# Performance work log

Hardware: AMD Instinct MI355X
Metric: run time of the kernel (lower is better)

Reference implementation:

```python
import jax, jax.numpy as jnp
import numpy as np

H = 1024        # hidden_size
NH = 16         # num heads
HD = H // NH    # head dim = 64
B, S = 2, 2048


def _linear_params(key, fan_in, fan_out):
    k1, k2 = jax.random.split(key)
    bound = 1.0 / np.sqrt(fan_in)
    w = jax.random.uniform(k1, (fan_in, fan_out), jnp.float32, -bound, bound)
    b = jax.random.uniform(k2, (fan_out,), jnp.float32, -bound, bound)
    return w, b


def setup_inputs() -> dict:
    key = jax.random.key(0)
    ks = jax.random.split(key, 10)
    hidden_states = jax.random.normal(ks[0], (B, S, H), jnp.float32)
    topic_states = jax.random.normal(ks[1], (B, H), jnp.float32)
    attention_mask = jnp.zeros((B, 1, 1, S), jnp.float32)
    Wq, bq = _linear_params(ks[2], H, H)
    Wk, bk = _linear_params(ks[3], H, H)
    Wv, bv = _linear_params(ks[4], H, H)
    Wtp, btp = _linear_params(ks[5], H, H)
    Wta, bta = _linear_params(ks[6], H, H)
    Wd, bd = _linear_params(ks[7], H, H)
    ln_g = jnp.ones((H,), jnp.float32)
    ln_b = jnp.zeros((H,), jnp.float32)
    return {
        "hidden_states": hidden_states, "topic_states": topic_states,
        "attention_mask": attention_mask,
        "Wq": Wq, "bq": bq, "Wk": Wk, "bk": bk, "Wv": Wv, "bv": bv,
        "Wtp": Wtp, "btp": btp, "Wta": Wta, "bta": bta,
        "Wd": Wd, "bd": bd, "ln_g": ln_g, "ln_b": ln_b,
    }


def reference(hidden_states, topic_states, attention_mask,
              Wq, bq, Wk, bk, Wv, bv, Wtp, btp, Wta, bta, Wd, bd, ln_g, ln_b):
    # topic gating: two linears on [B,H], broadcast over seq
    topic_proj = topic_states @ Wtp + btp
    topic_att = topic_proj @ Wta + bta                     # [B,H]
    gate = jax.nn.sigmoid(topic_att)[:, None, :]           # [B,1,H]

    q = hidden_states @ Wq + bq                            # [B,S,H]
    k = (hidden_states @ Wk + bk) * gate                   # sigmoid-gated keys
    v = hidden_states @ Wv + bv

    def split_heads(x):  # [B,S,H] -> [B,NH,S,HD]
        return x.reshape(B, S, NH, HD).transpose(0, 2, 1, 3)

    qh, kh, vh = split_heads(q), split_heads(k), split_heads(v)

    scores = jnp.einsum('bhqd,bhkd->bhqk', qh, kh) / np.sqrt(HD).astype(np.float32)
    scores = scores + attention_mask                       # additive mask
    probs = jax.nn.softmax(scores, axis=-1)                # dropout = identity (eval)
    ctx = jnp.einsum('bhqk,bhkd->bhqd', probs, vh)
    ctx = ctx.transpose(0, 2, 1, 3).reshape(B, S, H)

    out = ctx @ Wd + bd                                    # dense + (eval) dropout
    x = out + hidden_states                                # residual
    mu = jnp.mean(x, axis=-1, keepdims=True)
    var = jnp.mean(jnp.square(x - mu), axis=-1, keepdims=True)
    return (x - mu) * jax.lax.rsqrt(var + 1e-5) * ln_g + ln_b
```

## Files before the change

kernel.cpp:

```cpp
#include <hip/hip_runtime.h>

typedef unsigned short u16;
typedef unsigned int   u32;
typedef __attribute__((ext_vector_type(4)))  float f32x4;
typedef __attribute__((ext_vector_type(16))) float f32x16;
typedef __attribute__((ext_vector_type(8)))  __bf16 bf16x8;
typedef __attribute__((ext_vector_type(8)))  u16  u16x8;
typedef __attribute__((ext_vector_type(4)))  u16  u16x4;

#define HDIM 1024
#define SEQ  2048
#define NB   2
#define MROWS 4096
#define QSCALE 0.18033688011111793f
#define LOG2E  1.4426950408889634f
#define TOPK 64
#define TOPC 16

__device__ __forceinline__ u16 f2bf(float f) {
  u32 u = __float_as_uint(f);
  u32 r = u + 0x7FFFu + ((u >> 16) & 1u);
  return (u16)(r >> 16);
}

__device__ __forceinline__ u32 pkbf(float a, float b) {
  union { __bf16 h[2]; u32 w; } u;
  u.h[0] = (__bf16)a; u.h[1] = (__bf16)b;
  return u.w;
}

__device__ __forceinline__ void gload_lds16(const void* gp, void* lp) {
  __builtin_amdgcn_global_load_lds(
      (const __attribute__((address_space(1))) void*)gp,
      (__attribute__((address_space(3))) void*)lp, 16, 0, 0);
}

__global__ void wt_bf16_kernel(const float* __restrict__ w0, const float* __restrict__ w1,
                               const float* __restrict__ w2, const float* __restrict__ w3,
                               u16* __restrict__ out) {
  const float* W = (blockIdx.z == 0) ? w0 : (blockIdx.z == 1) ? w1 : (blockIdx.z == 2) ? w2 : w3;
  u16* Wt = out + (size_t)blockIdx.z * HDIM * HDIM;
  __shared__ float t[32][33];
  const int k0 = blockIdx.x * 32, n0 = blockIdx.y * 32;
  const int tx = threadIdx.x, ty = threadIdx.y;
#pragma unroll
  for (int j = 0; j < 32; j += 8)
    t[ty + j][tx] = W[(size_t)(k0 + ty + j) * HDIM + n0 + tx];
  __syncthreads();
#pragma unroll
  for (int j = 0; j < 32; j += 8)
    Wt[(size_t)(n0 + ty + j) * HDIM + k0 + tx] = f2bf(t[tx][ty + j]);
}

__global__ void cvt_bf16_kernel(const float* __restrict__ in, u16* __restrict__ out) {
  const size_t i = (size_t)blockIdx.x * 256 + threadIdx.x;
  f32x4 v = *(const f32x4*)(in + i * 4);
  u16x4 o;
#pragma unroll
  for (int e = 0; e < 4; ++e) o[e] = f2bf(v[e]);
  *(u16x4*)(out + i * 4) = o;
}

__global__ void topic_partial_kernel(const float* __restrict__ in, const float* __restrict__ W,
                                     float* __restrict__ part) {
  const int c = blockIdx.x;
  const int b = blockIdx.y;
  const int t = threadIdx.x;
  const float* inb = in + b * HDIM + c * TOPK;
  f32x4 acc = {};
#pragma unroll 8
  for (int k = 0; k < TOPK; ++k) {
    const f32x4 w4 = *(const f32x4*)(W + (size_t)(c * TOPK + k) * HDIM + t * 4);
    acc += inb[k] * w4;
  }
  *(f32x4*)(part + ((size_t)(b * TOPC + c)) * HDIM + t * 4) = acc;
}

__global__ void topic_reduce_kernel(const float* __restrict__ part, const float* __restrict__ bias,
                                    float* __restrict__ out, int sigmoid_mode) {
  const int b = blockIdx.y;
  const int n = blockIdx.x * 256 + threadIdx.x;
  float s = bias[n];
#pragma unroll
  for (int c = 0; c < TOPC; ++c) s += part[((size_t)(b * TOPC + c)) * HDIM + n];
  out[b * HDIM + n] = sigmoid_mode ? (1.f / (1.f + __expf(-s))) : s;
}

template <int MODE>
__global__ __launch_bounds__(256, 2)
void gemm_kernel(const u16* __restrict__ A, const u16* __restrict__ Wt,
                 const float* __restrict__ b0, const float* __restrict__ b1,
                 const float* __restrict__ b2, const float* __restrict__ gate,
                 const float* __restrict__ resid,
                 u16* __restrict__ outb, float* __restrict__ outf) {
  const int n0 = blockIdx.x * 128;
  const int m0 = blockIdx.y * 128;
  const int z = blockIdx.z;
  const u16* W = Wt + (size_t)z * (HDIM * HDIM);
  const float* bias = (MODE == 0) ? (z == 0 ? b0 : (z == 1 ? b1 : b2)) : b0;

  __shared__ __align__(16) u16 Alds[128 * 64];
  __shared__ __align__(16) u16 Blds[128 * 64];

  const int tid = threadIdx.x;
  const int lane = tid & 63;
  const int w = tid >> 6;
  const int wm = w >> 1, wn = w & 1;
  const int srow = tid >> 3, sslot = tid & 7;

  f32x4 acc[4][4] = {};

  for (int k0 = 0; k0 < HDIM; k0 += 64) {
    __syncthreads();
#pragma unroll
    for (int j = 0; j < 4; ++j) {
      const int row = j * 32 + srow;
      const int gs = (sslot ^ (row & 7)) * 8;
      gload_lds16(A + (size_t)(m0 + row) * HDIM + k0 + gs, Alds + j * 2048 + w * 512);
      gload_lds16(W + (size_t)(n0 + row) * HDIM + k0 + gs, Blds + j * 2048 + w * 512);
    }
    __syncthreads();
#pragma unroll
    for (int kk = 0; kk < 2; ++kk) {
      const int slot = ((((kk << 2) + (lane >> 4)) ^ (lane & 7)) << 3);
      bf16x8 af[4], bfr[4];
#pragma unroll
      for (int i = 0; i < 4; ++i) {
        af[i]  = *(const bf16x8*)(&Alds[(wm * 64 + i * 16 + (lane & 15)) * 64 + slot]);
        bfr[i] = *(const bf16x8*)(&Blds[(wn * 64 + i * 16 + (lane & 15)) * 64 + slot]);
      }
#pragma unroll
      for (int i = 0; i < 4; ++i)
#pragma unroll
        for (int jn = 0; jn < 4; ++jn)
          acc[i][jn] = __builtin_amdgcn_mfma_f32_16x16x32_bf16(af[i], bfr[jn], acc[i][jn], 0, 0, 0);
    }
  }

  const int rbase = (lane >> 4) << 2;
#pragma unroll
  for (int i = 0; i < 4; ++i) {
#pragma unroll
    for (int jn = 0; jn < 4; ++jn) {
      const int n = n0 + wn * 64 + jn * 16 + (lane & 15);
      const float bv = bias[n];
#pragma unroll
      for (int r = 0; r < 4; ++r) {
        const int m = m0 + wm * 64 + i * 16 + rbase + r;
        float v = acc[i][jn][r] + bv;
        if (MODE == 0) {
          if (z == 0) v *= QSCALE;
          if (z == 1) v *= gate[(m >> 11) * HDIM + n];
          outb[(size_t)z * MROWS * HDIM + (size_t)m * HDIM + n] = f2bf(v);
        } else {
          v += resid[(size_t)m * HDIM + n];
          outf[(size_t)m * HDIM + n] = v;
        }
      }
    }
  }
}

__global__ __launch_bounds__(256, 2)
void attn_kernel(const u16* __restrict__ Q, const u16* __restrict__ K,
                 const u16* __restrict__ V, const float* __restrict__ mask,
                 u16* __restrict__ O) {
  const int q0 = blockIdx.x * 128;
  const int h = blockIdx.y;
  const int b = blockIdx.z;
  const size_t base = ((size_t)b * SEQ) * HDIM + h * 64;
  const int tid = threadIdx.x, lane = tid & 63, w = tid >> 6;
  const int hh = lane >> 5;
  const int ql = lane & 31;
  const int srow = tid >> 3, sslot = tid & 7;

  __shared__ __align__(16) u16 Kss[2][64 * 64];
  __shared__ __align__(16) u16 Vts[2][64 * 64];

  bf16x8 Qf[4];
  {
    const u16* qp = Q + base + (size_t)(q0 + w * 32 + ql) * HDIM;
#pragma unroll
    for (int ds = 0; ds < 4; ++ds)
      Qf[ds] = *(const bf16x8*)(qp + ds * 16 + hh * 8);
  }

  float m_run = -1e30f, l_run = 0.f;
  f32x16 accA = {}, accB = {};

  {
#pragma unroll
    for (int c = 0; c < 2; ++c) {
      const int i2 = c * 4 + w;
      const int row = i2 * 8 + (lane >> 3);
      const int sl = lane & 7;
      gload_lds16(K + base + (size_t)row * HDIM + ((sl ^ (row & 7)) * 8),
                  &Kss[0][i2 * 512]);
    }
    u16x8 vr[2];
#pragma unroll
    for (int jj = 0; jj < 2; ++jj)
      vr[jj] = *(const u16x8*)(V + base + (size_t)(jj * 32 + srow) * HDIM + sslot * 8);
#pragma unroll
    for (int jj = 0; jj < 2; ++jj) {
      const int kr = jj * 32 + srow;
#pragma unroll
      for (int e = 0; e < 8; ++e) {
        const int d = sslot * 8 + e;
        Vts[0][d * 64 + ((((kr >> 3) ^ (d & 7) ^ ((d >> 3) & 7))) << 3) + (kr & 7)] = vr[jj][e];
      }
    }
  }
  __syncthreads();

  for (int t = 0; t < SEQ / 64; ++t) {
    const int cur = t & 1;
    const int kvt0 = t * 64;
    u16x8 vr[2];
    if (t + 1 < SEQ / 64) {
#pragma unroll
      for (int jj = 0; jj < 2; ++jj)
        vr[jj] = *(const u16x8*)(V + base + (size_t)(kvt0 + 64 + jj * 32 + srow) * HDIM + sslot * 8);
#pragma unroll
      for (int c = 0; c < 2; ++c) {
        const int i2 = c * 4 + w;
        const int row = i2 * 8 + (lane >> 3);
        const int sl = lane & 7;
        gload_lds16(K + base + (size_t)(kvt0 + 64 + row) * HDIM + ((sl ^ (row & 7)) * 8),
                    &Kss[cur ^ 1][i2 * 512]);
      }
    }

    f32x16 sv[2] = {{}, {}};
    __builtin_amdgcn_s_setprio(1);
#pragma unroll
    for (int ds = 0; ds < 4; ++ds) {
      const int xo = (((ds * 2 + hh) ^ (ql & 7)) << 3);
      const bf16x8 kf0 = *(const bf16x8*)(&Kss[cur][(ql) * 64 + xo]);
      const bf16x8 kf1 = *(const bf16x8*)(&Kss[cur][(32 + ql) * 64 + xo]);
      sv[0] = __builtin_amdgcn_mfma_f32_32x32x16_bf16(kf0, Qf[ds], sv[0], 0, 0, 0);
      sv[1] = __builtin_amdgcn_mfma_f32_32x32x16_bf16(kf1, Qf[ds], sv[1], 0, 0, 0);
    }
    __builtin_amdgcn_s_setprio(0);

    f32x4 m4[2][4];
    {
      const float* mrow = mask + (size_t)b * SEQ + kvt0 + hh * 4;
#pragma unroll
      for (int g = 0; g < 4; ++g) {
        m4[0][g] = *(const f32x4*)(mrow + g * 8);
        m4[1][g] = *(const f32x4*)(mrow + 32 + g * 8);
      }
    }
    f32x16 s_[2];
#pragma unroll
    for (int kvb = 0; kvb < 2; ++kvb)
#pragma unroll
      for (int j = 0; j < 16; ++j)
        s_[kvb][j] = fmaf(m4[kvb][j >> 2][j & 3], LOG2E, sv[kvb][j]);

    float t8[8];
#pragma unroll
    for (int j = 0; j < 8; ++j)
      t8[j] = fmaxf(fmaxf(s_[0][j], s_[0][j + 8]), fmaxf(s_[1][j], s_[1][j + 8]));
    float t4a = fmaxf(t8[0], t8[1]), t4b = fmaxf(t8[2], t8[3]);
    float t4c = fmaxf(t8[4], t8[5]), t4d = fmaxf(t8[6], t8[7]);
    float mx = fmaxf(fmaxf(t4a, t4b), fmaxf(t4c, t4d));
    mx = fmaxf(mx, __shfl_xor(mx, 32));

    if (!__all(mx <= m_run + 8.f)) {
      const float mnew = fmaxf(m_run, mx);
      const float corr = __builtin_amdgcn_exp2f(m_run - mnew);
      m_run = mnew;
      l_run *= corr;
#pragma unroll
      for (int j = 0; j < 16; ++j) {
        const float cj = __shfl(corr, (j & 3) + 8 * (j >> 2) + 4 * hh);
        accA[j] *= cj; accB[j] *= cj;
      }
    }

    f32x16 p_[2];
#pragma unroll
    for (int kvb = 0; kvb < 2; ++kvb)
#pragma unroll
      for (int j = 0; j < 16; ++j)
        p_[kvb][j] = __builtin_amdgcn_exp2f(s_[kvb][j] - m_run);
    {
      float r8[8];
#pragma unroll
      for (int j = 0; j < 8; ++j)
        r8[j] = (p_[0][j] + p_[0][j + 8]) + (p_[1][j] + p_[1][j + 8]);
      float ra = (r8[0] + r8[1]) + (r8[2] + r8[3]);
      float rb = (r8[4] + r8[5]) + (r8[6] + r8[7]);
      float rs = ra + rb;
      rs += __shfl_xor(rs, 32);
      l_run += rs;
    }

    __builtin_amdgcn_s_setprio(1);
#pragma unroll
    for (int kvb = 0; kvb < 2; ++kvb) {
#pragma unroll
      for (int s2 = 0; s2 < 2; ++s2) {
        const u32 a0 = pkbf(p_[kvb][s2 * 8 + 0], p_[kvb][s2 * 8 + 1]);
        const u32 a1 = pkbf(p_[kvb][s2 * 8 + 2], p_[kvb][s2 * 8 + 3]);
        const u32 b0v = pkbf(p_[kvb][s2 * 8 + 4], p_[kvb][s2 * 8 + 5]);
        const u32 b1v = pkbf(p_[kvb][s2 * 8 + 6], p_[kvb][s2 * 8 + 7]);
        const u32 sd0 = hh ? a0 : b0v, sd1 = hh ? a1 : b1v;
        const u32 r0 = (u32)__shfl_xor((int)sd0, 32);
        const u32 r1 = (u32)__shfl_xor((int)sd1, 32);
        union { u32 u[4]; bf16x8 v; } pu;
        pu.u[0] = hh ? r0 : a0;  pu.u[1] = hh ? r1 : a1;
        pu.u[2] = hh ? b0v : r0; pu.u[3] = hh ? b1v : r1;
        const int ks = kvb * 4 + s2 * 2 + hh;
#pragma unroll
        for (int dt = 0; dt < 2; ++dt) {
          const int d = dt * 32 + ql;
          const bf16x8 vf = *(const bf16x8*)(
              &Vts[cur][d * 64 + ((ks ^ (d & 7) ^ ((d >> 3) & 7)) << 3)]);
          if (dt == 0) accA = __builtin_amdgcn_mfma_f32_32x32x16_bf16(pu.v, vf, accA, 0, 0, 0);
          else         accB = __builtin_amdgcn_mfma_f32_32x32x16_bf16(pu.v, vf, accB, 0, 0, 0);
        }
      }
    }
    __builtin_amdgcn_s_setprio(0);

    if (t + 1 < SEQ / 64) {
#pragma unroll
      for (int jj = 0; jj < 2; ++jj) {
        const int kr = jj * 32 + srow;
#pragma unroll
        for (int e = 0; e < 8; ++e) {
          const int d = sslot * 8 + e;
          Vts[cur ^ 1][d * 64 + ((((kr >> 3) ^ (d & 7) ^ ((d >> 3) & 7))) << 3) + (kr & 7)] = vr[jj][e];
        }
      }
    }
    __syncthreads();
  }

  const float linv = 1.f / l_run;
#pragma unroll
  for (int j = 0; j < 16; ++j) {
    const int rq = (j & 3) + 8 * (j >> 2) + 4 * hh;
    const float lj = __shfl(linv, rq);
    const size_t orow = base + (size_t)(q0 + w * 32 + rq) * HDIM;
    O[orow + ql]      = f2bf(accA[j] * lj);
    O[orow + 32 + ql] = f2bf(accB[j] * lj);
  }
}

__global__ void ln_kernel(const float* __restrict__ x, const float* __restrict__ g,
                          const float* __restrict__ bb, float* __restrict__ out) {
  const int row = blockIdx.x;
  const int tid = threadIdx.x;
  const f32x4 v = *(const f32x4*)(x + (size_t)row * HDIM + tid * 4);
  float s = v[0] + v[1] + v[2] + v[3];
  float s2 = v[0] * v[0] + v[1] * v[1] + v[2] * v[2] + v[3] * v[3];
#pragma unroll
  for (int o = 1; o < 64; o <<= 1) { s += __shfl_xor(s, o); s2 += __shfl_xor(s2, o); }
  __shared__ float rs[4], rs2[4];
  if ((tid & 63) == 0) { rs[tid >> 6] = s; rs2[tid >> 6] = s2; }
  __syncthreads();
  s = rs[0] + rs[1] + rs[2] + rs[3];
  s2 = rs2[0] + rs2[1] + rs2[2] + rs2[3];
  const float mu = s * (1.f / HDIM);
  const float var = s2 * (1.f / HDIM) - mu * mu;
  const float inv = rsqrtf(var + 1e-5f);
  f32x4 o4;
#pragma unroll
  for (int e = 0; e < 4; ++e) {
    const int c = tid * 4 + e;
    o4[e] = (v[e] - mu) * inv * g[c] + bb[c];
  }
  *(f32x4*)(out + (size_t)row * HDIM + tid * 4) = o4;
}

extern "C" void kernel_launch(void* const* d_in, const int* in_sizes, int n_in,
                              void* d_out, int out_size, void* d_ws, size_t ws_size,
                              hipStream_t stream) {
  const float* hidden = (const float*)d_in[0];
  const float* topic  = (const float*)d_in[1];
  const float* mask   = (const float*)d_in[2];
  const float* Wq  = (const float*)d_in[3];  const float* bq  = (const float*)d_in[4];
  const float* Wk  = (const float*)d_in[5];  const float* bk  = (const float*)d_in[6];
  const float* Wv  = (const float*)d_in[7];  const float* bv  = (const float*)d_in[8];
  const float* Wtp = (const float*)d_in[9];  const float* btp = (const float*)d_in[10];
  const float* Wta = (const float*)d_in[11]; const float* bta = (const float*)d_in[12];
  const float* Wd  = (const float*)d_in[13]; const float* bd  = (const float*)d_in[14];
  const float* lng = (const float*)d_in[15]; const float* lnb = (const float*)d_in[16];
  float* out = (float*)d_out;

  char* ws = (char*)d_ws;
  u16* hs_bf  = (u16*)(ws);
  u16* WtAll  = (u16*)(ws + (size_t)(8u << 20));
  u16* qkv    = (u16*)(ws + (size_t)(16u << 20));
  u16* ctx    = (u16*)(ws + (size_t)(40u << 20));
  float* xbuf = (float*)(ws + (size_t)(16u << 20));
  float* tproj = (float*)(ws + (size_t)(48u << 20));
  float* tgate = (float*)(ws + (size_t)(48u << 20) + 8192);
  float* tpart = (float*)(ws + (size_t)(16u << 20));

  wt_bf16_kernel<<<dim3(32, 32, 4), dim3(32, 8), 0, stream>>>(Wq, Wk, Wv, Wd, WtAll);
  cvt_bf16_kernel<<<4096, 256, 0, stream>>>(hidden, hs_bf);
  topic_partial_kernel<<<dim3(TOPC, NB), 256, 0, stream>>>(topic, Wtp, tpart);
  topic_reduce_kernel<<<dim3(4, NB), 256, 0, stream>>>(tpart, btp, tproj, 0);
  topic_partial_kernel<<<dim3(TOPC, NB), 256, 0, stream>>>(tproj, Wta, tpart);
  topic_reduce_kernel<<<dim3(4, NB), 256, 0, stream>>>(tpart, bta, tgate, 1);
  gemm_kernel<0><<<dim3(8, 32, 3), 256, 0, stream>>>(hs_bf, WtAll, bq, bk, bv, tgate,
                                                     nullptr, qkv, nullptr);
  attn_kernel<<<dim3(16, 16, NB), 256, 0, stream>>>(qkv, qkv + (size_t)MROWS * HDIM,
                                                    qkv + 2 * (size_t)MROWS * HDIM, mask, ctx);
  gemm_kernel<1><<<dim3(8, 32, 1), 256, 0, stream>>>(ctx, WtAll + 3 * (size_t)HDIM * HDIM,
                                                     bd, nullptr, nullptr, nullptr, hidden,
                                                     nullptr, xbuf);
  ln_kernel<<<4096, 256, 0, stream>>>(xbuf, lng, lnb, out);
}
```

Before: 165.4 us.

## Split attention KV range in two with a combine kernel for more blocks

The attention kernel gains a SPLIT template mode that processes half of the key/value sequence per block, doubling the grid from 512 to 1024 blocks. Each block writes unnormalized fp32 accumulators and running max/sum to workspace, and a new combine kernel merges the two halves and emits the bf16 context. The change also raises launch bounds to 4 blocks per CU and drops the setprio hints. It aims to fill more of the GPU's compute units, at the cost of extra fp32 partial traffic (about 32 MB written and read back), one more launch, and possible register spills under the tighter launch bound. The split path only runs when the workspace is at least 81 MB.

```diff
diff --git a/kernel.cpp b/kernel.cpp
--- a/kernel.cpp
+++ b/kernel.cpp
@@ -3,6 +3,7 @@
 typedef unsigned short u16;
 typedef unsigned int   u32;
 typedef __attribute__((ext_vector_type(4)))  float f32x4;
+typedef __attribute__((ext_vector_type(2)))  float f32x2;
 typedef __attribute__((ext_vector_type(16))) float f32x16;
 typedef __attribute__((ext_vector_type(8)))  __bf16 bf16x8;
 typedef __attribute__((ext_vector_type(8)))  u16  u16x8;
@@ -161,13 +162,18 @@
   }
 }
 
-__global__ __launch_bounds__(256, 2)
+template <int SPLIT>
+__global__ __launch_bounds__(256, 4)
 void attn_kernel(const u16* __restrict__ Q, const u16* __restrict__ K,
                  const u16* __restrict__ V, const float* __restrict__ mask,
-                 u16* __restrict__ O) {
+                 u16* __restrict__ O, float* __restrict__ pacc, float* __restrict__ pml) {
   const int q0 = blockIdx.x * 128;
   const int h = blockIdx.y;
-  const int b = blockIdx.z;
+  const int zz = blockIdx.z;
+  const int b = SPLIT ? (zz % NB) : zz;
+  const int half = SPLIT ? (zz / NB) : 0;
+  const int kvs = half * (SEQ / 2);
+  const int NT = SPLIT ? (SEQ / 128) : (SEQ / 64);
   const size_t base = ((size_t)b * SEQ) * HDIM + h * 64;
   const int tid = threadIdx.x, lane = tid & 63, w = tid >> 6;
   const int hh = lane >> 5;
@@ -194,13 +200,13 @@
       const int i2 = c * 4 + w;
       const int row = i2 * 8 + (lane >> 3);
       const int sl = lane & 7;
-      gload_lds16(K + base + (size_t)row * HDIM + ((sl ^ (row & 7)) * 8),
+      gload_lds16(K + base + (size_t)(kvs + row) * HDIM + ((sl ^ (row & 7)) * 8),
                   &Kss[0][i2 * 512]);
     }
     u16x8 vr[2];
 #pragma unroll
     for (int jj = 0; jj < 2; ++jj)
-      vr[jj] = *(const u16x8*)(V + base + (size_t)(jj * 32 + srow) * HDIM + sslot * 8);
+      vr[jj] = *(const u16x8*)(V + base + (size_t)(kvs + jj * 32 + srow) * HDIM + sslot * 8);
 #pragma unroll
     for (int jj = 0; jj < 2; ++jj) {
       const int kr = jj * 32 + srow;
@@ -213,11 +219,11 @@
   }
   __syncthreads();
 
-  for (int t = 0; t < SEQ / 64; ++t) {
+  for (int t = 0; t < NT; ++t) {
     const int cur = t & 1;
-    const int kvt0 = t * 64;
+    const int kvt0 = kvs + t * 64;
     u16x8 vr[2];
-    if (t + 1 < SEQ / 64) {
+    if (t + 1 < NT) {
 #pragma unroll
       for (int jj = 0; jj < 2; ++jj)
         vr[jj] = *(const u16x8*)(V + base + (size_t)(kvt0 + 64 + jj * 32 + srow) * HDIM + sslot * 8);
@@ -232,7 +238,6 @@
     }
 
     f32x16 sv[2] = {{}, {}};
-    __builtin_amdgcn_s_setprio(1);
 #pragma unroll
     for (int ds = 0; ds < 4; ++ds) {
       const int xo = (((ds * 2 + hh) ^ (ql & 7)) << 3);
@@ -241,7 +246,6 @@
       sv[0] = __builtin_amdgcn_mfma_f32_32x32x16_bf16(kf0, Qf[ds], sv[0], 0, 0, 0);
       sv[1] = __builtin_amdgcn_mfma_f32_32x32x16_bf16(kf1, Qf[ds], sv[1], 0, 0, 0);
     }
-    __builtin_amdgcn_s_setprio(0);
 
     f32x4 m4[2][4];
     {
@@ -298,7 +302,6 @@
       l_run += rs;
     }
 
-    __builtin_amdgcn_s_setprio(1);
 #pragma unroll
     for (int kvb = 0; kvb < 2; ++kvb) {
 #pragma unroll
@@ -324,9 +327,8 @@
         }
       }
     }
-    __builtin_amdgcn_s_setprio(0);
-
-    if (t + 1 < SEQ / 64) {
+
+    if (t + 1 < NT) {
 #pragma unroll
       for (int jj = 0; jj < 2; ++jj) {
         const int kr = jj * 32 + srow;
@@ -340,15 +342,53 @@
     __syncthreads();
   }
 
-  const float linv = 1.f / l_run;
-#pragma unroll
-  for (int j = 0; j < 16; ++j) {
-    const int rq = (j & 3) + 8 * (j >> 2) + 4 * hh;
-    const float lj = __shfl(linv, rq);
-    const size_t orow = base + (size_t)(q0 + w * 32 + rq) * HDIM;
-    O[orow + ql]      = f2bf(accA[j] * lj);
-    O[orow + 32 + ql] = f2bf(accB[j] * lj);
-  }
+  if (SPLIT) {
+#pragma unroll
+    for (int j = 0; j < 16; ++j) {
+      const int rq = (j & 3) + 8 * (j >> 2) + 4 * hh;
+      const size_t orow = ((size_t)(half * NB + b) * SEQ + q0 + w * 32 + rq) * HDIM + h * 64;
+      pacc[orow + ql]      = accA[j];
+      pacc[orow + 32 + ql] = accB[j];
+    }
+    if (hh == 0) {
+      const size_t mli = (((size_t)half * NB + b) * 16 + h) * SEQ + q0 + w * 32 + ql;
+      *(f32x2*)(pml + mli * 2) = f32x2{m_run, l_run};
+    }
+  } else {
+    const float linv = 1.f / l_run;
+#pragma unroll
+    for (int j = 0; j < 16; ++j) {
+      const int rq = (j & 3) + 8 * (j >> 2) + 4 * hh;
+      const float lj = __shfl(linv, rq);
+      const size_t orow = base + (size_t)(q0 + w * 32 + rq) * HDIM;
+      O[orow + ql]      = f2bf(accA[j] * lj);
+      O[orow + 32 + ql] = f2bf(accB[j] * lj);
+    }
+  }
+}
+
+__global__ void attn_combine_kernel(const float* __restrict__ pacc, const float* __restrict__ pml,
+                                    u16* __restrict__ ctx) {
+  const size_t gid = (size_t)blockIdx.x * 256 + threadIdx.x;
+  const size_t e0 = gid * 4;
+  const size_t row = e0 >> 10;
+  const int col = (int)(e0 & 1023);
+  const int h = col >> 6;
+  const size_t b = row >> 11, s = row & 2047;
+  const size_t mli0 = ((b) * 16 + h) * SEQ + s;
+  const size_t mli1 = (((size_t)NB + b) * 16 + h) * SEQ + s;
+  const f32x2 ml0 = *(const f32x2*)(pml + mli0 * 2);
+  const f32x2 ml1 = *(const f32x2*)(pml + mli1 * 2);
+  const float mstar = fmaxf(ml0[0], ml1[0]);
+  const float w0 = __builtin_amdgcn_exp2f(ml0[0] - mstar);
+  const float w1 = __builtin_amdgcn_exp2f(ml1[0] - mstar);
+  const float inv = 1.f / (ml0[1] * w0 + ml1[1] * w1);
+  const f32x4 a0 = *(const f32x4*)(pacc + row * HDIM + col);
+  const f32x4 a1 = *(const f32x4*)(pacc + ((size_t)NB * SEQ) * HDIM + row * HDIM + col);
+  u16x4 o;
+#pragma unroll
+  for (int e = 0; e < 4; ++e) o[e] = f2bf((a0[e] * w0 + a1[e] * w1) * inv);
+  *(u16x4*)(ctx + row * HDIM + col) = o;
 }
 
 __global__ void ln_kernel(const float* __restrict__ x, const float* __restrict__ g,
@@ -401,6 +441,9 @@
   float* tproj = (float*)(ws + (size_t)(48u << 20));
   float* tgate = (float*)(ws + (size_t)(48u << 20) + 8192);
   float* tpart = (float*)(ws + (size_t)(16u << 20));
+  float* pacc  = (float*)(ws + (size_t)(48u << 20));
+  float* pml   = (float*)(ws + (size_t)(80u << 20));
+  const bool split = ws_size >= ((size_t)81 << 20);
 
   wt_bf16_kernel<<<dim3(32, 32, 4), dim3(32, 8), 0, stream>>>(Wq, Wk, Wv, Wd, WtAll);
   cvt_bf16_kernel<<<4096, 256, 0, stream>>>(hidden, hs_bf);
@@ -410,8 +453,14 @@
   topic_reduce_kernel<<<dim3(4, NB), 256, 0, stream>>>(tpart, bta, tgate, 1);
   gemm_kernel<0><<<dim3(8, 32, 3), 256, 0, stream>>>(hs_bf, WtAll, bq, bk, bv, tgate,
                                                      nullptr, qkv, nullptr);
-  attn_kernel<<<dim3(16, 16, NB), 256, 0, stream>>>(qkv, qkv + (size_t)MROWS * HDIM,
-                                                    qkv + 2 * (size_t)MROWS * HDIM, mask, ctx);
+  if (split) {
+    attn_kernel<1><<<dim3(16, 16, NB * 2), 256, 0, stream>>>(
+        qkv, qkv + (size_t)MROWS * HDIM, qkv + 2 * (size_t)MROWS * HDIM, mask, ctx, pacc, pml);
+    attn_combine_kernel<<<4096, 256, 0, stream>>>(pacc, pml, ctx);
+  } else {
+    attn_kernel<0><<<dim3(16, 16, NB), 256, 0, stream>>>(
+        qkv, qkv + (size_t)MROWS * HDIM, qkv + 2 * (size_t)MROWS * HDIM, mask, ctx, nullptr, nullptr);
+  }
   gemm_kernel<1><<<dim3(8, 32, 1), 256, 0, stream>>>(ctx, WtAll + 3 * (size_t)HDIM * HDIM,
                                                      bd, nullptr, nullptr, nullptr, hidden,
                                                      nullptr, xbuf);
```

After: 228.6 us. 1.38x slower.
